# Kernel tuning notes

Hardware: AMD Instinct MI355X
Metric: run time of the kernel (lower is better)

Reference implementation:

```python
import jax, jax.numpy as jnp
import numpy as np

B, L, D, K = 32, 512, 512, 3
LOG_2PI = float(np.log(2.0 * np.pi))


def conv1d(x, w, b):
    # x: (B, L, 1), w: (D, 1, K), b: (D,) -> (B, L, D); padding = (K-1)//2
    pad = (w.shape[-1] - 1) // 2
    y = jax.lax.conv_general_dilated(
        x.transpose(0, 2, 1), w, window_strides=(1,), padding=[(pad, pad)],
        dimension_numbers=('NCH', 'OIH', 'NCH'))
    return y.transpose(0, 2, 1) + b


def setup_inputs() -> dict:
    ks = jax.random.split(jax.random.key(0), 14)
    x = jax.random.normal(ks[0], (B, L, D), dtype=jnp.float32)
    durations_float = jax.random.uniform(ks[1], (B, L), dtype=jnp.float32) * 8.0
    durations_int = jax.random.randint(ks[2], (B, L), 1, 8, dtype=jnp.int32)
    energies = jax.random.normal(ks[3], (B, L), dtype=jnp.float32)
    pitch = jax.random.normal(ks[4], (B, L), dtype=jnp.float32)
    input_lengths = jax.random.randint(ks[5], (B,), L // 2, L + 1, dtype=jnp.int32)
    input_lengths = input_lengths.at[0].set(L)  # ensure max length == L (torch masks at max(lengths))
    s = 0.05
    w_dur = jax.random.normal(ks[6], (D, 1, K), dtype=jnp.float32) * s
    b_dur = jax.random.normal(ks[7], (D,), dtype=jnp.float32) * s
    w_en = jax.random.normal(ks[8], (D, 1, K), dtype=jnp.float32) * s
    b_en = jax.random.normal(ks[9], (D,), dtype=jnp.float32) * s
    w_pitch = jax.random.normal(ks[10], (D, 1, K), dtype=jnp.float32) * s
    b_pitch = jax.random.normal(ks[11], (D,), dtype=jnp.float32) * s
    w_lin = jax.random.normal(ks[12], (1, D), dtype=jnp.float32) * s
    b_lin = jax.random.normal(ks[13], (1,), dtype=jnp.float32) * s
    nb_frames = int(jnp.max(jnp.cumsum(durations_int, axis=1)))  # concrete static T
    return dict(x=x, durations_float=durations_float, durations_int=durations_int,
                energies=energies, pitch=pitch, input_lengths=input_lengths,
                w_dur=w_dur, b_dur=b_dur, w_en=w_en, b_en=b_en,
                w_pitch=w_pitch, b_pitch=b_pitch, w_lin=w_lin, b_lin=b_lin,
                nb_frames=nb_frames)


def reference(x, durations_float, durations_int, energies, pitch, input_lengths,
              w_dur, b_dur, w_en, b_en, w_pitch, b_pitch, w_lin, b_lin, nb_frames):
    Bb, Ll, Dd = x.shape
    dur_e = conv1d(durations_float[..., None], w_dur, b_dur)   # (B, L, D)
    en_e = conv1d(energies[..., None], w_en, b_en)
    pi_e = conv1d(pitch[..., None], w_pitch, b_pitch)
    x = x + en_e + pi_e
    range_inputs = x + dur_e
    ranges = jax.nn.softplus(range_inputs @ w_lin.T + b_lin)[..., 0]  # (B, L)
    valid = jnp.arange(Ll) < input_lengths[:, None]                   # (B, L) True = valid
    ranges = jnp.where(valid, ranges, 1.0)
    d = durations_int.astype(x.dtype)
    cumsum = jnp.cumsum(durations_int, axis=1)
    means = d * 0.5 + jnp.concatenate(
        [jnp.zeros((Bb, 1), x.dtype), cumsum[:, :-1].astype(x.dtype)], axis=1)  # (B, L)
    frames = jnp.arange(nb_frames, dtype=x.dtype) + 0.5                # (T,)
    z = (frames[None, None, :] - means[..., None]) / ranges[..., None] # (B, L, T)
    log_probs = -0.5 * z * z - jnp.log(ranges)[..., None] - 0.5 * LOG_2PI
    probs = jnp.where(valid[..., None], jnp.exp(log_probs), 0.0)       # (B, L, T)
    weights = probs / (jnp.sum(probs, axis=1, keepdims=True) + 1e-20)
    # torch: sum_L x[b,l,d] * w[b,l,t] -> (B, D, T), then permute -> (B, T, D)
    x_upsamp = jnp.einsum('bld,blt->btd', x, weights)
    return x_upsamp, weights
```

## Files before the change

### kernel.cpp

```cpp
#include <hip/hip_runtime.h>
#include <hip/hip_bf16.h>
#include <stdint.h>

#define NB 32
#define NL 512
#define ND 512

typedef __bf16 bf16x8 __attribute__((ext_vector_type(8)));
typedef float  f32x4  __attribute__((ext_vector_type(4)));

__device__ __forceinline__ unsigned short f2bf(float f) {
    uint32_t u = __float_as_uint(f);
    u = (u + 0x7fffu + ((u >> 16) & 1u)) >> 16;
    return (unsigned short)u;
}


__global__ __launch_bounds__(256) void fuse2_kernel(
    const float* __restrict__ x, const float* __restrict__ df,
    const float* __restrict__ en, const float* __restrict__ pi,
    const int* __restrict__ lens,
    const float* __restrict__ w_dur, const float* __restrict__ b_dur,
    const float* __restrict__ w_en,  const float* __restrict__ b_en,
    const float* __restrict__ w_pi,  const float* __restrict__ b_pi,
    const float* __restrict__ w_lin, const float* __restrict__ b_lin,
    unsigned short* __restrict__ Xb, float* __restrict__ ranges)
{
    const int blk = blockIdx.x;
    const int b   = blk >> 6;
    const int lb  = (blk & 63) << 3;
    const int tid = threadIdx.x;
    const int d0  = tid << 1;

    float we[2][3], wp[2][3], wd[2][3], bev[2], bpv[2], bdv[2], wl[2];
    #pragma unroll
    for (int q = 0; q < 2; ++q) {
        const int d = d0 + q;
        #pragma unroll
        for (int k = 0; k < 3; ++k) {
            we[q][k] = w_en[d*3+k];
            wp[q][k] = w_pi[d*3+k];
            wd[q][k] = w_dur[d*3+k];
        }
        bev[q] = b_en[d]; bpv[q] = b_pi[d]; bdv[q] = b_dur[d]; wl[q] = w_lin[d];
    }

    float acc[8];
    #pragma unroll
    for (int i = 0; i < 8; ++i) acc[i] = 0.f;

    uint4 chunk[2];
    unsigned short* cu = (unsigned short*)chunk;

    #pragma unroll
    for (int li = 0; li < 8; ++li) {
        const int l  = lb + li;
        const int bl = (b << 9) + l;
        const float dm1 = (l > 0)      ? df[bl-1] : 0.f;
        const float dc  = df[bl];
        const float dp1 = (l < NL-1)   ? df[bl+1] : 0.f;
        const float em1 = (l > 0)      ? en[bl-1] : 0.f;
        const float ec  = en[bl];
        const float ep1 = (l < NL-1)   ? en[bl+1] : 0.f;
        const float pm1 = (l > 0)      ? pi[bl-1] : 0.f;
        const float pc  = pi[bl];
        const float pp1 = (l < NL-1)   ? pi[bl+1] : 0.f;
        const float2 xv = *(const float2*)&x[(size_t)bl * ND + d0];
        #pragma unroll
        for (int q = 0; q < 2; ++q) {
            const float ev  = we[q][0]*em1 + we[q][1]*ec + we[q][2]*ep1 + bev[q];
            const float pv  = wp[q][0]*pm1 + wp[q][1]*pc + wp[q][2]*pp1 + bpv[q];
            const float xxv = (q ? xv.y : xv.x) + ev + pv;
            cu[q*8 + li] = f2bf(xxv);
            const float dv  = wd[q][0]*dm1 + wd[q][1]*dc + wd[q][2]*dp1 + bdv[q];
            acc[li] += (xxv + dv) * wl[q];
        }
    }
    #pragma unroll
    for (int q = 0; q < 2; ++q) {
        const int d = d0 + q;
        const size_t off = (size_t)b * (NL * ND)
            + (size_t)(((lb >> 5) << 5) + (d >> 4)) * 512
            + (size_t)((((lb >> 3) & 3) << 4) + (d & 15)) * 8;
        *(uint4*)&Xb[off] = chunk[q];
    }

    #pragma unroll
    for (int li = 0; li < 8; ++li)
        #pragma unroll
        for (int off = 32; off; off >>= 1)
            acc[li] += __shfl_down(acc[li], off, 64);
    __shared__ float red[4][8];
    const int lane = tid & 63, wid = tid >> 6;
    if (lane == 0)
        #pragma unroll
        for (int li = 0; li < 8; ++li) red[wid][li] = acc[li];
    __syncthreads();
    if (tid < 8) {
        const float s = red[0][tid] + red[1][tid] + red[2][tid] + red[3][tid] + b_lin[0];
        float r = fmaxf(s, 0.f) + log1pf(expf(-fabsf(s)));
        if (lb + tid >= lens[b]) r = 1.0f;
        ranges[(b << 9) + lb + tid] = r;
    }
}


#define C2F 0.84932180028801904272f

#define STAGE_X2(kk, buf) do {                                                  \
    const char* src_ = Bbase + (size_t)(kk) * 32768;                            \
    char* dst_ = smem + (buf) * 32768;                                          \
    _Pragma("unroll")                                                           \
    for (int c = 0; c < 4; ++c) {                                               \
        const int o_ = (wid * 4 + c) * 1024;                                    \
        __builtin_amdgcn_global_load_lds(                                       \
            (__attribute__((address_space(1))) void*)(src_ + o_ + lane * 16),   \
            (__attribute__((address_space(3))) void*)(dst_ + o_), 16, 0, 0);    \
    }                                                                           \
} while (0)

#define GENP2(kk, buf) do {                                                     \
    const int l0_ = (kk) * 32 + oct * 4;                                        \
    float pv_[4];                                                               \
    unsigned short pu_[4];                                                      \
    _Pragma("unroll")                                                           \
    for (int j = 0; j < 4; ++j) {                                               \
        const float u_ = fmaf(ftv, t_a[l0_ + j], t_b[l0_ + j]);                 \
        pv_[j] = t_sc[l0_ + j] * exp2f(-u_ * u_);                               \
        pu_[j] = f2bf(pv_[j]);                                                  \
    }                                                                           \
    char* pd_ = smem + 65536 + (buf) * 4096 + (tloc >> 4) * 1024                \
              + (((oct >> 1) << 4) + (tloc & 15)) * 16 + ((oct & 1) << 3);      \
    *(uint2*)pd_ = *(uint2*)pu_;                                                \
    if (tvalid) {                                                               \
        _Pragma("unroll")                                                       \
        for (int j = 0; j < 4; ++j)                                             \
            woutb[(size_t)(l0_ + j) * T] = pv_[j] * myDinv;                     \
    }                                                                           \
} while (0)

__global__ __launch_bounds__(512, 4) void fusedwg4_kernel(
    const unsigned short* __restrict__ Xb,
    const float* __restrict__ ranges, const int* __restrict__ di,
    const int* __restrict__ lens,
    float* __restrict__ wout, float* __restrict__ xup, int T)
{
    __shared__ __align__(16) char smem[80128];
    float* t_a   = (float*)(smem + 73728);
    float* t_b   = (float*)(smem + 75776);
    float* t_sc  = (float*)(smem + 77824);
    float* dinvL = (float*)(smem + 79872);
    int*   scanA = (int*)(smem + 65536);
    int*   scanB = (int*)(smem + 67584);
    float* partial = (float*)(smem + 69632);

    const int tid  = threadIdx.x;
    const int lane = tid & 63, wid = tid >> 6;
    const int wn   = wid;

    const int i    = blockIdx.x;
    const int xcd  = i & 7, slot = i >> 3;
    const int b    = (xcd << 2) + (slot & 3);
    const int m    = slot >> 2;
    const int m64  = m << 6;

    const int tloc = tid & 63;
    const int oct  = tid >> 6;
    const int tglb = m64 + tloc;
    const bool tvalid = tglb < T;
    const float ftv = (float)tglb + 0.5f;

    const char* Bbase = (const char*)Xb + (size_t)b * (NL * ND * 2);

    STAGE_X2(0, 0);

    const int dv = di[(b << 9) + tid];
    scanA[tid] = dv;
    __syncthreads();
    {
        int* src = scanA; int* dst = scanB;
        #pragma unroll
        for (int off = 1; off < NL; off <<= 1) {
            dst[tid] = src[tid] + (tid >= off ? src[tid - off] : 0);
            __syncthreads();
            int* tmp = src; src = dst; dst = tmp;
        }
        const float mu = (float)src[tid] - 0.5f * (float)dv;
        const float r  = ranges[(b << 9) + tid];
        const float inv = 1.f / r;
        t_a[tid]  = inv * C2F;
        t_b[tid]  = -mu * inv * C2F;
        t_sc[tid] = (tid < lens[b]) ? 0.3989422804014327f * inv : 0.f;
    }
    __syncthreads();

    {
        float s = 0.f;
        const int lbeg = oct << 6;
        #pragma unroll 4
        for (int l = lbeg; l < lbeg + 64; ++l) {
            const float u = fmaf(ftv, t_a[l], t_b[l]);
            s += t_sc[l] * exp2f(-u * u);
        }
        partial[(oct << 6) + tloc] = s;
    }
    __syncthreads();
    if (tid < 64) {
        float sum = 0.f;
        #pragma unroll
        for (int o = 0; o < 8; ++o) sum += partial[(o << 6) + tid];
        dinvL[tid] = 1.f / (sum + 1e-20f);
    }
    __syncthreads();
    const float myDinv = dinvL[tloc];
    float* woutb = wout + (size_t)(b << 9) * T + tglb;

    f32x4 acc[4][4];
    #pragma unroll
    for (int ii = 0; ii < 4; ++ii)
        #pragma unroll
        for (int jj = 0; jj < 4; ++jj) acc[ii][jj] = (f32x4){0.f, 0.f, 0.f, 0.f};

    GENP2(0, 0);

    for (int k = 0; k < 16; ++k) {
        asm volatile("s_waitcnt vmcnt(4) lgkmcnt(0)" ::: "memory");
        __builtin_amdgcn_s_barrier();
        __builtin_amdgcn_sched_barrier(0);
        const int cur = k & 1;
        if (k < 15) {
            STAGE_X2(k + 1, cur ^ 1);
            __builtin_amdgcn_sched_barrier(0);
            GENP2(k + 1, cur ^ 1);
        }
        bf16x8 af[4], bfr[4];
        #pragma unroll
        for (int ii = 0; ii < 4; ++ii)
            af[ii] = *(const bf16x8*)(smem + 65536 + cur * 4096 + ii * 1024 + lane * 16);
        #pragma unroll
        for (int jj = 0; jj < 4; ++jj)
            bfr[jj] = *(const bf16x8*)(smem + cur * 32768 + ((wn << 2) + jj) * 1024 + lane * 16);
        #pragma unroll
        for (int ii = 0; ii < 4; ++ii)
            #pragma unroll
            for (int jj = 0; jj < 4; ++jj)
                acc[ii][jj] = __builtin_amdgcn_mfma_f32_16x16x32_bf16(af[ii], bfr[jj], acc[ii][jj], 0, 0, 0);
    }

    float* lf = (float*)smem;
    float* Ob = xup + (size_t)b * T * ND;
    #pragma unroll
    for (int c = 0; c < 4; ++c) {
        __syncthreads();
        #pragma unroll
        for (int jj = 0; jj < 4; ++jj)
            #pragma unroll
            for (int r = 0; r < 4; ++r) {
                const int row = ((lane >> 4) << 2) + r;
                const int col = (wn << 6) + (jj << 4) + (lane & 15);
                lf[row * 516 + col] = acc[c][jj][r];
            }
        __syncthreads();
        const int trow = tid >> 7;
        const int colq = (tid & 127) << 2;
        #pragma unroll
        for (int s = 0; s < 4; ++s) {
            const int row = trow + (s << 2);
            const int t = m64 + (c << 4) + row;
            if (t < T) {
                const float dsc = dinvL[(c << 4) + row];
                f32x4 v = *(const f32x4*)(lf + row * 516 + colq);
                v[0] *= dsc; v[1] *= dsc; v[2] *= dsc; v[3] *= dsc;
                *(f32x4*)&Ob[(size_t)t * ND + colq] = v;
            }
        }
    }
}

__global__ __launch_bounds__(512) void means_kernel(
    const int* __restrict__ di, float* __restrict__ means)
{
    const int b = blockIdx.x;
    const int l = threadIdx.x;
    __shared__ int s[NL];
    const int d = di[b * NL + l];
    s[l] = d;
    __syncthreads();
    #pragma unroll
    for (int off = 1; off < NL; off <<= 1) {
        const int v = (l >= off) ? s[l - off] : 0;
        __syncthreads();
        s[l] += v;
        __syncthreads();
    }
    means[b * NL + l] = 0.5f * (float)d + (float)(s[l] - d);
}

__global__ __launch_bounds__(256) void fuse_kernel(
    const float* __restrict__ x, const float* __restrict__ df,
    const float* __restrict__ en, const float* __restrict__ pi,
    const int* __restrict__ lens,
    const float* __restrict__ w_dur, const float* __restrict__ b_dur,
    const float* __restrict__ w_en,  const float* __restrict__ b_en,
    const float* __restrict__ w_pi,  const float* __restrict__ b_pi,
    const float* __restrict__ w_lin, const float* __restrict__ b_lin,
    float* __restrict__ xx, float* __restrict__ ranges)
{
    const int bl = blockIdx.x;
    const int b  = bl >> 9;
    const int l  = bl & (NL - 1);
    const int tid = threadIdx.x;
    const float dm1 = (l > 0)      ? df[bl - 1] : 0.f;
    const float d0  = df[bl];
    const float dp1 = (l < NL - 1) ? df[bl + 1] : 0.f;
    const float em1 = (l > 0)      ? en[bl - 1] : 0.f;
    const float e0  = en[bl];
    const float ep1 = (l < NL - 1) ? en[bl + 1] : 0.f;
    const float pm1 = (l > 0)      ? pi[bl - 1] : 0.f;
    const float p0  = pi[bl];
    const float pp1 = (l < NL - 1) ? pi[bl + 1] : 0.f;
    float acc = 0.f;
    #pragma unroll
    for (int d = tid; d < ND; d += 256) {
        const float xv = x[(size_t)bl * ND + d];
        const float ev = w_en[d*3]*em1 + w_en[d*3+1]*e0 + w_en[d*3+2]*ep1 + b_en[d];
        const float pv = w_pi[d*3]*pm1 + w_pi[d*3+1]*p0 + w_pi[d*3+2]*pp1 + b_pi[d];
        const float xxv = xv + ev + pv;
        xx[(size_t)bl * ND + d] = xxv;
        const float dv = w_dur[d*3]*dm1 + w_dur[d*3+1]*d0 + w_dur[d*3+2]*dp1 + b_dur[d];
        acc += (xxv + dv) * w_lin[d];
    }
    #pragma unroll
    for (int off = 32; off; off >>= 1) acc += __shfl_down(acc, off, 64);
    __shared__ float red[4];
    const int lane = tid & 63, wid = tid >> 6;
    if (lane == 0) red[wid] = acc;
    __syncthreads();
    if (tid == 0) {
        const float s = red[0] + red[1] + red[2] + red[3] + b_lin[0];
        float r = fmaxf(s, 0.f) + log1pf(expf(-fabsf(s)));
        if (l >= lens[b]) r = 1.0f;
        ranges[bl] = r;
    }
}

__global__ __launch_bounds__(256) void weights_kernel(
    const float* __restrict__ ranges, const float* __restrict__ means,
    const int* __restrict__ lens, float* __restrict__ weights, int T)
{
    const int b = blockIdx.y;
    const int t = blockIdx.x * 256 + threadIdx.x;
    __shared__ float sm[NL], sinv[NL], sc[NL];
    const int len = lens[b];
    for (int l = threadIdx.x; l < NL; l += 256) {
        const float r = ranges[b * NL + l];
        const float inv = 1.f / r;
        sm[l] = means[b * NL + l];
        sinv[l] = inv;
        sc[l] = (l < len) ? 0.3989422804014327f * inv : 0.f;
    }
    __syncthreads();
    if (t >= T) return;
    const float ft = (float)t + 0.5f;
    float sum = 0.f;
    #pragma unroll 4
    for (int l = 0; l < NL; ++l) {
        const float z = (ft - sm[l]) * sinv[l];
        sum += sc[l] * __expf(-0.5f * z * z);
    }
    const float dinv = 1.f / (sum + 1e-20f);
    #pragma unroll 4
    for (int l = 0; l < NL; ++l) {
        const float z = (ft - sm[l]) * sinv[l];
        weights[((size_t)b * NL + l) * T + t] = sc[l] * __expf(-0.5f * z * z) * dinv;
    }
}

#define BM 64
#define BN 64
#define BK 16
__global__ __launch_bounds__(256) void gemm_f32_kernel(
    const float* __restrict__ xx, const float* __restrict__ weights,
    float* __restrict__ out, int T)
{
    const int b  = blockIdx.z;
    const int t0 = blockIdx.y * BM;
    const int d0 = blockIdx.x * BN;
    const float* __restrict__ W = weights + (size_t)b * NL * T;
    const float* __restrict__ X = xx + (size_t)b * NL * ND;
    float* __restrict__ O = out + (size_t)b * T * ND;
    __shared__ float As[BK][BM];
    __shared__ float Bs[BK][BN];
    const int tid = threadIdx.x;
    const int tx = tid & 15;
    const int ty = tid >> 4;
    const int lr = tid >> 4;
    const int lc = (tid & 15) * 4;
    const bool vec_ok = (t0 + BM <= T) && ((T & 3) == 0);
    float acc[4][4] = {};
    for (int l0 = 0; l0 < NL; l0 += BK) {
        if (vec_ok) {
            *(float4*)&As[lr][lc] = *(const float4*)&W[(size_t)(l0 + lr) * T + t0 + lc];
        } else {
            #pragma unroll
            for (int j = 0; j < 4; ++j) {
                const int tcol = t0 + lc + j;
                As[lr][lc + j] = (tcol < T) ? W[(size_t)(l0 + lr) * T + tcol] : 0.f;
            }
        }
        *(float4*)&Bs[lr][lc] = *(const float4*)&X[(size_t)(l0 + lr) * ND + d0 + lc];
        __syncthreads();
        #pragma unroll
        for (int k = 0; k < BK; ++k) {
            float a[4], bb[4];
            *(float4*)a  = *(const float4*)&As[k][ty * 4];
            *(float4*)bb = *(const float4*)&Bs[k][tx * 4];
            #pragma unroll
            for (int i = 0; i < 4; ++i)
                #pragma unroll
                for (int j = 0; j < 4; ++j)
                    acc[i][j] += a[i] * bb[j];
        }
        __syncthreads();
    }
    #pragma unroll
    for (int i = 0; i < 4; ++i) {
        const int t = t0 + ty * 4 + i;
        if (t < T)
            *(float4*)&O[(size_t)t * ND + d0 + tx * 4] =
                make_float4(acc[i][0], acc[i][1], acc[i][2], acc[i][3]);
    }
}

extern "C" void kernel_launch(void* const* d_in, const int* in_sizes, int n_in,
                              void* d_out, int out_size, void* d_ws, size_t ws_size,
                              hipStream_t stream) {
    const float* x     = (const float*)d_in[0];
    const float* df    = (const float*)d_in[1];
    const int*   di    = (const int*)  d_in[2];
    const float* en    = (const float*)d_in[3];
    const float* pi    = (const float*)d_in[4];
    const int*   lens  = (const int*)  d_in[5];
    const float* w_dur = (const float*)d_in[6];
    const float* b_dur = (const float*)d_in[7];
    const float* w_en  = (const float*)d_in[8];
    const float* b_en  = (const float*)d_in[9];
    const float* w_pi  = (const float*)d_in[10];
    const float* b_pi  = (const float*)d_in[11];
    const float* w_lin = (const float*)d_in[12];
    const float* b_lin = (const float*)d_in[13];

    const int B = NB, L = NL, D = ND;
    const int T = out_size / (B * (L + D));
    const int MT = (T + 63) / 64;

    float* xup  = (float*)d_out;
    float* wout = xup + (size_t)B * T * D;

    const size_t XbBytes = (size_t)B * L * D * 2;
    const size_t need = XbBytes + (size_t)B * L * sizeof(float);

    if (ws_size >= need) {
        unsigned short* Xb = (unsigned short*)d_ws;
        float* ranges = (float*)(Xb + (size_t)B * L * D);

        hipLaunchKernelGGL(fuse2_kernel, dim3(B * 64), dim3(256), 0, stream,
                           x, df, en, pi, lens, w_dur, b_dur, w_en, b_en,
                           w_pi, b_pi, w_lin, b_lin, Xb, ranges);
        hipLaunchKernelGGL(fusedwg4_kernel, dim3(MT * 32), dim3(512), 0, stream,
                           Xb, ranges, di, lens, wout, xup, T);
    } else {
        float* xx     = (float*)d_ws;
        float* ranges = xx + (size_t)B * L * D;
        float* means  = ranges + (size_t)B * L;
        hipLaunchKernelGGL(fuse_kernel, dim3(B * L), dim3(256), 0, stream,
                           x, df, en, pi, lens, w_dur, b_dur, w_en, b_en,
                           w_pi, b_pi, w_lin, b_lin, xx, ranges);
        hipLaunchKernelGGL(means_kernel, dim3(B), dim3(512), 0, stream, di, means);
        hipLaunchKernelGGL(weights_kernel, dim3((T + 255) / 256, B), dim3(256), 0, stream,
                           ranges, means, lens, wout, T);
        hipLaunchKernelGGL(gemm_f32_kernel, dim3(D / BN, (T + BM - 1) / BM, B), dim3(256), 0, stream,
                           xx, wout, xup, T);
    }
}
```

Before: 105.1 us.

## Load X tiles directly into registers instead of staging through LDS

```diff
diff --git a/kernel.cpp b/kernel.cpp
--- a/kernel.cpp
+++ b/kernel.cpp
@@ -107,19 +107,7 @@
 
 #define C2F 0.84932180028801904272f
 
-#define STAGE_X2(kk, buf) do {                                                  \
-    const char* src_ = Bbase + (size_t)(kk) * 32768;                            \
-    char* dst_ = smem + (buf) * 32768;                                          \
-    _Pragma("unroll")                                                           \
-    for (int c = 0; c < 4; ++c) {                                               \
-        const int o_ = (wid * 4 + c) * 1024;                                    \
-        __builtin_amdgcn_global_load_lds(                                       \
-            (__attribute__((address_space(1))) void*)(src_ + o_ + lane * 16),   \
-            (__attribute__((address_space(3))) void*)(dst_ + o_), 16, 0, 0);    \
-    }                                                                           \
-} while (0)
-
-#define GENP2(kk, buf) do {                                                     \
+#define GENP5(kk, buf) do {                                                     \
     const int l0_ = (kk) * 32 + oct * 4;                                        \
     float pv_[4];                                                               \
     unsigned short pu_[4];                                                      \
@@ -129,7 +117,7 @@
         pv_[j] = t_sc[l0_ + j] * exp2f(-u_ * u_);                               \
         pu_[j] = f2bf(pv_[j]);                                                  \
     }                                                                           \
-    char* pd_ = smem + 65536 + (buf) * 4096 + (tloc >> 4) * 1024                \
+    char* pd_ = smem + (buf) * 4096 + (tloc >> 4) * 1024                        \
               + (((oct >> 1) << 4) + (tloc & 15)) * 16 + ((oct & 1) << 3);      \
     *(uint2*)pd_ = *(uint2*)pu_;                                                \
     if (tvalid) {                                                               \
@@ -139,20 +127,20 @@
     }                                                                           \
 } while (0)
 
-__global__ __launch_bounds__(512, 4) void fusedwg4_kernel(
+__global__ __launch_bounds__(512, 4) void fusedwg5_kernel(
     const unsigned short* __restrict__ Xb,
     const float* __restrict__ ranges, const int* __restrict__ di,
     const int* __restrict__ lens,
     float* __restrict__ wout, float* __restrict__ xup, int T)
 {
-    __shared__ __align__(16) char smem[80128];
-    float* t_a   = (float*)(smem + 73728);
-    float* t_b   = (float*)(smem + 75776);
-    float* t_sc  = (float*)(smem + 77824);
-    float* dinvL = (float*)(smem + 79872);
-    int*   scanA = (int*)(smem + 65536);
-    int*   scanB = (int*)(smem + 67584);
-    float* partial = (float*)(smem + 69632);
+    __shared__ __align__(16) char smem[39424];
+    float* t_a   = (float*)(smem + 33024);
+    float* t_b   = (float*)(smem + 35072);
+    float* t_sc  = (float*)(smem + 37120);
+    float* dinvL = (float*)(smem + 39168);
+    int*   scanA = (int*)smem;
+    int*   scanB = (int*)(smem + 2048);
+    float* partial = (float*)(smem + 4096);
 
     const int tid  = threadIdx.x;
     const int lane = tid & 63, wid = tid >> 6;
@@ -170,9 +158,13 @@
     const bool tvalid = tglb < T;
     const float ftv = (float)tglb + 0.5f;
 
-    const char* Bbase = (const char*)Xb + (size_t)b * (NL * ND * 2);
-
-    STAGE_X2(0, 0);
+    const char* Bbase = (const char*)Xb + (size_t)b * (NL * ND * 2)
+                      + (size_t)(wn << 2) * 1024 + lane * 16;
+
+    bf16x8 bxc[4], bxn[4];
+    #pragma unroll
+    for (int jj = 0; jj < 4; ++jj)
+        bxc[jj] = *(const bf16x8*)(Bbase + jj * 1024);
 
     const int dv = di[(b << 9) + tid];
     scanA[tid] = dv;
@@ -221,30 +213,31 @@
         #pragma unroll
         for (int jj = 0; jj < 4; ++jj) acc[ii][jj] = (f32x4){0.f, 0.f, 0.f, 0.f};
 
-    GENP2(0, 0);
-
+    GENP5(0, 0);
+
+    #pragma unroll
     for (int k = 0; k < 16; ++k) {
-        asm volatile("s_waitcnt vmcnt(4) lgkmcnt(0)" ::: "memory");
+        asm volatile("s_waitcnt lgkmcnt(0)" ::: "memory");
         __builtin_amdgcn_s_barrier();
         __builtin_amdgcn_sched_barrier(0);
         const int cur = k & 1;
         if (k < 15) {
-            STAGE_X2(k + 1, cur ^ 1);
-            __builtin_amdgcn_sched_barrier(0);
-            GENP2(k + 1, cur ^ 1);
-        }
-        bf16x8 af[4], bfr[4];
+            #pragma unroll
+            for (int jj = 0; jj < 4; ++jj)
+                bxn[jj] = *(const bf16x8*)(Bbase + (size_t)(k + 1) * 32768 + jj * 1024);
+            GENP5(k + 1, cur ^ 1);
+        }
+        bf16x8 af[4];
         #pragma unroll
         for (int ii = 0; ii < 4; ++ii)
-            af[ii] = *(const bf16x8*)(smem + 65536 + cur * 4096 + ii * 1024 + lane * 16);
-        #pragma unroll
-        for (int jj = 0; jj < 4; ++jj)
-            bfr[jj] = *(const bf16x8*)(smem + cur * 32768 + ((wn << 2) + jj) * 1024 + lane * 16);
+            af[ii] = *(const bf16x8*)(smem + cur * 4096 + ii * 1024 + lane * 16);
         #pragma unroll
         for (int ii = 0; ii < 4; ++ii)
             #pragma unroll
             for (int jj = 0; jj < 4; ++jj)
-                acc[ii][jj] = __builtin_amdgcn_mfma_f32_16x16x32_bf16(af[ii], bfr[jj], acc[ii][jj], 0, 0, 0);
+                acc[ii][jj] = __builtin_amdgcn_mfma_f32_16x16x32_bf16(af[ii], bxc[jj], acc[ii][jj], 0, 0, 0);
+        #pragma unroll
+        for (int jj = 0; jj < 4; ++jj) bxc[jj] = bxn[jj];
     }
 
     float* lf = (float*)smem;
@@ -467,7 +460,7 @@
         hipLaunchKernelGGL(fuse2_kernel, dim3(B * 64), dim3(256), 0, stream,
                            x, df, en, pi, lens, w_dur, b_dur, w_en, b_en,
                            w_pi, b_pi, w_lin, b_lin, Xb, ranges);
-        hipLaunchKernelGGL(fusedwg4_kernel, dim3(MT * 32), dim3(512), 0, stream,
+        hipLaunchKernelGGL(fusedwg5_kernel, dim3(MT * 32), dim3(512), 0, stream,
                            Xb, ranges, di, lens, wout, xup, T);
     } else {
         float* xx     = (float*)d_ws;
```

After: 98.94 us, median of 3. -5.8%, faster.
